# Kernel tuning notes

Hardware: AMD Instinct MI355X
Metric: run time of the kernel (lower is better)

Reference implementation:

```python
import jax, jax.numpy as jnp
import numpy as np

HIDDEN_DIM = 512
N = 2 * HIDDEN_DIM  # 1024
B, T_K = 32, 2048


def setup_inputs() -> dict:
    key = jax.random.key(0)
    ks = jax.random.split(key, 10)
    s_t_hat = jax.random.normal(ks[0], (B, N), dtype=jnp.float32)
    encoder_outputs = jax.random.normal(ks[1], (B, T_K, N), dtype=jnp.float32)
    encoder_feature = jax.random.normal(ks[2], (B * T_K, N), dtype=jnp.float32)
    stmt_feature = jax.random.uniform(ks[3], (B, T_K), dtype=jnp.float32) * 0.01
    enc_padding_mask = jnp.ones((B, T_K), dtype=jnp.float32)
    coverage = jax.random.uniform(ks[4], (B, T_K), dtype=jnp.float32)
    # learned params
    W_dec = jax.random.normal(ks[5], (N, N), dtype=jnp.float32) / np.sqrt(N)
    b_dec = jnp.zeros((N,), dtype=jnp.float32)
    v_w = jax.random.normal(ks[6], (N,), dtype=jnp.float32) / np.sqrt(N)
    W_c = jax.random.normal(ks[7], (N,), dtype=jnp.float32)  # Linear(1, N, bias=False)
    return {
        "s_t_hat": s_t_hat,
        "encoder_outputs": encoder_outputs,
        "encoder_feature": encoder_feature,
        "stmt_feature": stmt_feature,
        "enc_padding_mask": enc_padding_mask,
        "coverage": coverage,
        "W_dec": W_dec,
        "b_dec": b_dec,
        "v_w": v_w,
        "W_c": W_c,
    }


def reference(s_t_hat, encoder_outputs, encoder_feature, stmt_feature,
              enc_padding_mask, coverage, W_dec, b_dec, v_w, W_c):
    b, t_k, n = encoder_outputs.shape
    # decode_proj: [b, n]
    dec_fea = s_t_hat @ W_dec.T + b_dec
    # broadcast-add decoder feature + coverage feature (Linear(1, n) == outer product)
    att_features = (encoder_feature.reshape(b, t_k, n)
                    + dec_fea[:, None, :]
                    + coverage[:, :, None] * W_c)  # [b, t_k, n]
    e = jnp.tanh(att_features)
    scores = jnp.einsum('btn,n->bt', e, v_w)  # v: Linear(n, 1, bias=False)
    attn_dist_ = jax.nn.softmax(scores, axis=1) * enc_padding_mask
    attn_dist = attn_dist_ / attn_dist_.sum(axis=1, keepdims=True)
    attn_dist = attn_dist + stmt_feature * enc_padding_mask
    c_t = jnp.einsum('bt,btn->bn', attn_dist, encoder_outputs)  # bmm
    coverage_out = coverage + attn_dist
    return (c_t, attn_dist, coverage_out)
```

## Files before the change

### kernel.cpp

```cpp
#include <hip/hip_runtime.h>

#define B   32
#define TK  2048
#define N   1024
#define NF4 256

#define OUT_CT   0
#define OUT_ATTN (B * N)
#define OUT_COV  (B * N + B * TK)

__device__ __forceinline__ float hw_exp2(float x) {
    return __builtin_amdgcn_exp2f(x);
}

__device__ __forceinline__ float fast_tanh(float x) {
    float t = hw_exp2(x * 2.8853900817779268f);
    return 1.0f - 2.0f * __builtin_amdgcn_rcpf(t + 1.0f);
}

__device__ __forceinline__ float wave_reduce_sum(float v) {
#pragma unroll
    for (int off = 32; off > 0; off >>= 1) v += __shfl_xor(v, off, 64);
    return v;
}

__global__ __launch_bounds__(256) void decfea_kernel(
    const float4* __restrict__ S,
    const float4* __restrict__ W,
    const float*  __restrict__ bias,
    float*        __restrict__ dec)
{
    int w    = blockIdx.x * 4 + (threadIdx.x >> 6);
    int lane = threadIdx.x & 63;
    int n    = w >> 3;
    int b0   = (w & 7) * 4;

    float4 wr[4];
#pragma unroll
    for (int j = 0; j < 4; ++j) wr[j] = W[n * NF4 + j * 64 + lane];

#pragma unroll
    for (int i = 0; i < 4; ++i) {
        int b = b0 + i;
        float acc = 0.0f;
#pragma unroll
        for (int j = 0; j < 4; ++j) {
            float4 s4 = S[b * NF4 + j * 64 + lane];
            acc += s4.x * wr[j].x + s4.y * wr[j].y + s4.z * wr[j].z + s4.w * wr[j].w;
        }
        acc = wave_reduce_sum(acc);
        if (lane == 0) dec[b * N + n] = acc + bias[n];
    }
}

__global__ __launch_bounds__(256) void scores_kernel(
    const float4* __restrict__ EF,
    const float4* __restrict__ DEC,
    const float4* __restrict__ WC,
    const float4* __restrict__ VW,
    const float*  __restrict__ cov,
    float*        __restrict__ scores)
{
    int r    = blockIdx.x * 4 + (threadIdx.x >> 6);
    int lane = threadIdx.x & 63;
    int b    = r >> 11;
    float c  = cov[r];

    const float4* ef = EF + (size_t)r * NF4;
    const float4* de = DEC + b * NF4;

    float partial = 0.0f;
#pragma unroll
    for (int j = 0; j < 4; ++j) {
        int f = j * 64 + lane;
        float4 e  = ef[f];
        float4 d  = de[f];
        float4 wc = WC[f];
        float4 vw = VW[f];
        partial += fast_tanh(e.x + d.x + c * wc.x) * vw.x;
        partial += fast_tanh(e.y + d.y + c * wc.y) * vw.y;
        partial += fast_tanh(e.z + d.z + c * wc.z) * vw.z;
        partial += fast_tanh(e.w + d.w + c * wc.w) * vw.w;
    }
    partial = wave_reduce_sum(partial);
    if (lane == 0) scores[r] = partial;
}

__global__ __launch_bounds__(256) void softmax_kernel(
    const float* __restrict__ scores,
    const float* __restrict__ mask,
    const float* __restrict__ stmt,
    const float* __restrict__ coverage,
    float*       __restrict__ attn_ws,
    float*       __restrict__ out)
{
    int b = blockIdx.x, tid = threadIdx.x;
    __shared__ float red[256];

    float s[8];
    float m = -1e30f;
#pragma unroll
    for (int k = 0; k < 8; ++k) {
        s[k] = scores[b * TK + k * 256 + tid];
        m = fmaxf(m, s[k]);
    }
    red[tid] = m;
    __syncthreads();
    for (int step = 128; step > 0; step >>= 1) {
        if (tid < step) red[tid] = fmaxf(red[tid], red[tid + step]);
        __syncthreads();
    }
    float M = red[0];
    __syncthreads();

    float e[8];
    float loc = 0.0f;
#pragma unroll
    for (int k = 0; k < 8; ++k) {
        int t = k * 256 + tid;
        e[k] = hw_exp2((s[k] - M) * 1.4426950408889634f) * mask[b * TK + t];
        loc += e[k];
    }
    red[tid] = loc;
    __syncthreads();
    for (int step = 128; step > 0; step >>= 1) {
        if (tid < step) red[tid] += red[tid + step];
        __syncthreads();
    }
    float inv = 1.0f / red[0];

#pragma unroll
    for (int k = 0; k < 8; ++k) {
        int t = k * 256 + tid;
        int r = b * TK + t;
        float a = e[k] * inv + stmt[r] * mask[r];
        attn_ws[r] = a;
        out[OUT_ATTN + r] = a;
        out[OUT_COV + r] = coverage[r] + a;
    }

    float4 z = {0.0f, 0.0f, 0.0f, 0.0f};
    ((float4*)(out + OUT_CT))[b * NF4 + tid] = z;
}

__global__ __launch_bounds__(256) void ct_kernel(
    const float4* __restrict__ EO,
    const float*  __restrict__ attn,
    float*        __restrict__ ct)
{
    int s = blockIdx.x;
    int b = blockIdx.y;
    int tid = threadIdx.x;

    __shared__ float wbuf[128];
    if (tid < 128) wbuf[tid] = attn[b * TK + s * 128 + tid];
    __syncthreads();

    float4 acc = {0.0f, 0.0f, 0.0f, 0.0f};
    const float4* eo = EO + ((size_t)b * TK + s * 128) * NF4 + tid;
#pragma unroll 4
    for (int tt = 0; tt < 128; ++tt) {
        float w  = wbuf[tt];
        float4 v = eo[(size_t)tt * NF4];
        acc.x += w * v.x;
        acc.y += w * v.y;
        acc.z += w * v.z;
        acc.w += w * v.w;
    }
    float* dst = ct + b * N + tid * 4;
    atomicAdd(dst + 0, acc.x);
    atomicAdd(dst + 1, acc.y);
    atomicAdd(dst + 2, acc.z);
    atomicAdd(dst + 3, acc.w);
}

extern "C" void kernel_launch(void* const* d_in, const int* in_sizes, int n_in,
                              void* d_out, int out_size, void* d_ws, size_t ws_size,
                              hipStream_t stream) {
    const float* s_t_hat = (const float*)d_in[0];
    const float* EO      = (const float*)d_in[1];
    const float* EF      = (const float*)d_in[2];
    const float* stmt    = (const float*)d_in[3];
    const float* mask    = (const float*)d_in[4];
    const float* cov     = (const float*)d_in[5];
    const float* Wdec    = (const float*)d_in[6];
    const float* bdec    = (const float*)d_in[7];
    const float* vw      = (const float*)d_in[8];
    const float* wc      = (const float*)d_in[9];

    float* out = (float*)d_out;
    float* ws  = (float*)d_ws;
    float* dec    = ws;
    float* scores = ws + B * N;
    float* attn   = ws + B * N + B * TK;

    decfea_kernel<<<2048, 256, 0, stream>>>(
        (const float4*)s_t_hat, (const float4*)Wdec, bdec, dec);

    scores_kernel<<<16384, 256, 0, stream>>>(
        (const float4*)EF, (const float4*)dec, (const float4*)wc,
        (const float4*)vw, cov, scores);

    softmax_kernel<<<B, 256, 0, stream>>>(scores, mask, stmt, cov, attn, out);

    ct_kernel<<<dim3(16, B), 256, 0, stream>>>(
        (const float4*)EO, attn, out + OUT_CT);
}
```

Measured before the change: 524.7 us.

## Split context reduction into partial slices plus reduce, use nontemporal streaming loads

The context-vector pass now splits each batch's 2048 tokens across 32 slices instead of 16, doubling the blocks available to stream encoder_outputs. Partial sums go to workspace and a separate reduce kernel combines them, which replaces the float atomics and the zero-initialisation of c_t. Both big streaming reads (encoder_feature and encoder_outputs) use nontemporal loads, and each wave in the scores kernel now handles two rows to amortise the shared dec/Wc/v loads. The cost is one extra kernel launch and a partial-sum buffer written and read back through workspace.

```diff
diff --git a/kernel.cpp b/kernel.cpp
--- a/kernel.cpp
+++ b/kernel.cpp
@@ -9,6 +9,11 @@
 #define OUT_ATTN (B * N)
 #define OUT_COV  (B * N + B * TK)
 
+#define NSLICE 32
+#define TPS    (TK / NSLICE)
+
+typedef float v4f __attribute__((ext_vector_type(4)));
+
 __device__ __forceinline__ float hw_exp2(float x) {
     return __builtin_amdgcn_exp2f(x);
 }
@@ -22,6 +27,11 @@
 #pragma unroll
     for (int off = 32; off > 0; off >>= 1) v += __shfl_xor(v, off, 64);
     return v;
+}
+
+__device__ __forceinline__ float4 ldnt(const float4* p) {
+    v4f v = __builtin_nontemporal_load((const v4f*)p);
+    return make_float4(v.x, v.y, v.z, v.w);
 }
 
 __global__ __launch_bounds__(256) void decfea_kernel(
@@ -61,29 +71,41 @@
     const float*  __restrict__ cov,
     float*        __restrict__ scores)
 {
-    int r    = blockIdx.x * 4 + (threadIdx.x >> 6);
+    int w    = blockIdx.x * 4 + (threadIdx.x >> 6);
     int lane = threadIdx.x & 63;
-    int b    = r >> 11;
-    float c  = cov[r];
-
-    const float4* ef = EF + (size_t)r * NF4;
-    const float4* de = DEC + b * NF4;
-
-    float partial = 0.0f;
+    int r0   = w * 2;
+    int b    = r0 >> 11;
+    float c0 = cov[r0];
+    float c1 = cov[r0 + 1];
+
+    const float4* ef0 = EF + (size_t)r0 * NF4;
+    const float4* ef1 = ef0 + NF4;
+    const float4* de  = DEC + b * NF4;
+
+    float p0 = 0.0f, p1 = 0.0f;
 #pragma unroll
     for (int j = 0; j < 4; ++j) {
         int f = j * 64 + lane;
-        float4 e  = ef[f];
+        float4 e0 = ldnt(ef0 + f);
+        float4 e1 = ldnt(ef1 + f);
         float4 d  = de[f];
         float4 wc = WC[f];
         float4 vw = VW[f];
-        partial += fast_tanh(e.x + d.x + c * wc.x) * vw.x;
-        partial += fast_tanh(e.y + d.y + c * wc.y) * vw.y;
-        partial += fast_tanh(e.z + d.z + c * wc.z) * vw.z;
-        partial += fast_tanh(e.w + d.w + c * wc.w) * vw.w;
-    }
-    partial = wave_reduce_sum(partial);
-    if (lane == 0) scores[r] = partial;
+        p0 += fast_tanh(e0.x + d.x + c0 * wc.x) * vw.x;
+        p0 += fast_tanh(e0.y + d.y + c0 * wc.y) * vw.y;
+        p0 += fast_tanh(e0.z + d.z + c0 * wc.z) * vw.z;
+        p0 += fast_tanh(e0.w + d.w + c0 * wc.w) * vw.w;
+        p1 += fast_tanh(e1.x + d.x + c1 * wc.x) * vw.x;
+        p1 += fast_tanh(e1.y + d.y + c1 * wc.y) * vw.y;
+        p1 += fast_tanh(e1.z + d.z + c1 * wc.z) * vw.z;
+        p1 += fast_tanh(e1.w + d.w + c1 * wc.w) * vw.w;
+    }
+    p0 = wave_reduce_sum(p0);
+    p1 = wave_reduce_sum(p1);
+    if (lane == 0) {
+        scores[r0]     = p0;
+        scores[r0 + 1] = p1;
+    }
 }
 
 __global__ __launch_bounds__(256) void softmax_kernel(
@@ -91,7 +113,6 @@
     const float* __restrict__ mask,
     const float* __restrict__ stmt,
     const float* __restrict__ coverage,
-    float*       __restrict__ attn_ws,
     float*       __restrict__ out)
 {
     int b = blockIdx.x, tid = threadIdx.x;
@@ -134,44 +155,53 @@
         int t = k * 256 + tid;
         int r = b * TK + t;
         float a = e[k] * inv + stmt[r] * mask[r];
-        attn_ws[r] = a;
         out[OUT_ATTN + r] = a;
-        out[OUT_COV + r] = coverage[r] + a;
-    }
-
-    float4 z = {0.0f, 0.0f, 0.0f, 0.0f};
-    ((float4*)(out + OUT_CT))[b * NF4 + tid] = z;
-}
-
-__global__ __launch_bounds__(256) void ct_kernel(
+        out[OUT_COV + r]  = coverage[r] + a;
+    }
+}
+
+__global__ __launch_bounds__(256) void ct_partial_kernel(
     const float4* __restrict__ EO,
     const float*  __restrict__ attn,
-    float*        __restrict__ ct)
+    float4*       __restrict__ part)
 {
     int s = blockIdx.x;
     int b = blockIdx.y;
     int tid = threadIdx.x;
 
-    __shared__ float wbuf[128];
-    if (tid < 128) wbuf[tid] = attn[b * TK + s * 128 + tid];
+    __shared__ float wbuf[TPS];
+    if (tid < TPS) wbuf[tid] = attn[b * TK + s * TPS + tid];
     __syncthreads();
 
     float4 acc = {0.0f, 0.0f, 0.0f, 0.0f};
-    const float4* eo = EO + ((size_t)b * TK + s * 128) * NF4 + tid;
-#pragma unroll 4
-    for (int tt = 0; tt < 128; ++tt) {
+    const float4* eo = EO + ((size_t)b * TK + s * TPS) * NF4 + tid;
+#pragma unroll 8
+    for (int tt = 0; tt < TPS; ++tt) {
         float w  = wbuf[tt];
-        float4 v = eo[(size_t)tt * NF4];
+        float4 v = ldnt(eo + (size_t)tt * NF4);
         acc.x += w * v.x;
         acc.y += w * v.y;
         acc.z += w * v.z;
         acc.w += w * v.w;
     }
-    float* dst = ct + b * N + tid * 4;
-    atomicAdd(dst + 0, acc.x);
-    atomicAdd(dst + 1, acc.y);
-    atomicAdd(dst + 2, acc.z);
-    atomicAdd(dst + 3, acc.w);
+    part[((size_t)s * B + b) * NF4 + tid] = acc;
+}
+
+__global__ __launch_bounds__(256) void ct_reduce_kernel(
+    const float4* __restrict__ part,
+    float4*       __restrict__ ct)
+{
+    int i = blockIdx.x * 256 + threadIdx.x;
+    float4 acc = {0.0f, 0.0f, 0.0f, 0.0f};
+#pragma unroll
+    for (int s = 0; s < NSLICE; ++s) {
+        float4 v = part[(size_t)s * (B * NF4) + i];
+        acc.x += v.x;
+        acc.y += v.y;
+        acc.z += v.z;
+        acc.w += v.w;
+    }
+    ct[i] = acc;
 }
 
 extern "C" void kernel_launch(void* const* d_in, const int* in_sizes, int n_in,
@@ -192,17 +222,20 @@
     float* ws  = (float*)d_ws;
     float* dec    = ws;
     float* scores = ws + B * N;
-    float* attn   = ws + B * N + B * TK;
+    float* part   = ws + B * N + B * TK;
 
     decfea_kernel<<<2048, 256, 0, stream>>>(
         (const float4*)s_t_hat, (const float4*)Wdec, bdec, dec);
 
-    scores_kernel<<<16384, 256, 0, stream>>>(
+    scores_kernel<<<8192, 256, 0, stream>>>(
         (const float4*)EF, (const float4*)dec, (const float4*)wc,
         (const float4*)vw, cov, scores);
 
-    softmax_kernel<<<B, 256, 0, stream>>>(scores, mask, stmt, cov, attn, out);
-
-    ct_kernel<<<dim3(16, B), 256, 0, stream>>>(
-        (const float4*)EO, attn, out + OUT_CT);
-}
+    softmax_kernel<<<B, 256, 0, stream>>>(scores, mask, stmt, cov, out);
+
+    ct_partial_kernel<<<dim3(NSLICE, B), 256, 0, stream>>>(
+        (const float4*)EO, out + OUT_ATTN, (float4*)part);
+
+    ct_reduce_kernel<<<32, 256, 0, stream>>>(
+        (const float4*)part, (float4*)(out + OUT_CT));
+}
```

Measured after the change: 506.5 us. 3.5% less time.
